# Performance work log

Hardware: AMD Instinct MI355X
Metric: run time of the kernel (lower is better)

## Reference

```python
import jax, jax.numpy as jnp
import numpy as np

POOL_SIZE = 7  # matches init kwarg pool_size


def setup_inputs() -> dict:
    key = jax.random.key(0)
    k1, k2 = jax.random.split(key, 2)
    H, W, C, N = 50, 64, 1024, 1000
    stride = 16
    shared_layers = jax.random.normal(k1, (1, H, W, C), dtype=jnp.float32)
    # ROIs in image coordinates (y1, x1, y2, x2), image ~ (H*stride, W*stride)
    img_h, img_w = float(H * stride), float(W * stride)
    u = jax.random.uniform(k2, (N, 4), dtype=jnp.float32)
    y1 = u[:, 0] * (img_h * 0.6)
    x1 = u[:, 1] * (img_w * 0.6)
    y2 = y1 + 32.0 + u[:, 2] * (img_h * 0.4 - 32.0)
    x2 = x1 + 32.0 + u[:, 3] * (img_w * 0.4 - 32.0)
    rois = jnp.stack([y1, x1, y2, x2], axis=1)
    return {"shared_layers": shared_layers, "rois": rois, "extractor_stride": stride}


def _crop_and_resize(img, boxes, cs):
    """TF tf.image.crop_and_resize (bilinear, extrapolation_value=0) for a single image.
    img: [H, W, C]; boxes: [N, 4] normalized (y1, x1, y2, x2); cs: crop size (>1).
    Returns [N, cs, cs, C]."""
    H, W, C = img.shape
    y1, x1, y2, x2 = boxes[:, 0], boxes[:, 1], boxes[:, 2], boxes[:, 3]
    i = jnp.arange(cs, dtype=boxes.dtype)
    # sample coordinates in source pixel space: [N, cs]
    ys = y1[:, None] * (H - 1) + i[None, :] * ((y2 - y1) * (H - 1) / (cs - 1))[:, None]
    xs = x1[:, None] * (W - 1) + i[None, :] * ((x2 - x1) * (W - 1) / (cs - 1))[:, None]
    valid_y = (ys >= 0) & (ys <= H - 1)
    valid_x = (xs >= 0) & (xs <= W - 1)
    y0f = jnp.floor(ys)
    x0f = jnp.floor(xs)
    wy = (ys - y0f)[:, :, None, None]   # [N, cs, 1, 1]
    wx = (xs - x0f)[:, None, :, None]   # [N, 1, cs, 1]
    y0 = jnp.clip(y0f.astype(jnp.int32), 0, H - 1)
    y1i = jnp.clip(y0 + 1, 0, H - 1)
    x0 = jnp.clip(x0f.astype(jnp.int32), 0, W - 1)
    x1i = jnp.clip(x0 + 1, 0, W - 1)

    def gather(yi, xi):  # -> [N, cs, cs, C]
        return img[yi[:, :, None], xi[:, None, :]]

    top = gather(y0, x0) * (1.0 - wx) + gather(y0, x1i) * wx
    bot = gather(y1i, x0) * (1.0 - wx) + gather(y1i, x1i) * wx
    out = top * (1.0 - wy) + bot * wy
    mask = (valid_y[:, :, None] & valid_x[:, None, :])[..., None]
    return jnp.where(mask, out, jnp.zeros((), dtype=img.dtype))


def reference(shared_layers, rois, extractor_stride):
    rois = rois / jnp.asarray(extractor_stride, dtype=rois.dtype)
    H, W = shared_layers.shape[1], shared_layers.shape[2]
    # normalize (y1/h, x1/w, y2/h, x2/w)
    boxes = rois / jnp.array([H, W, H, W], dtype=rois.dtype)
    cs = POOL_SIZE * 2  # pre_pool_size
    crops = _crop_and_resize(shared_layers[0], boxes, cs)  # [N, 14, 14, C]
    N, C = crops.shape[0], crops.shape[-1]
    # MaxPooling2D pool 2x2 stride 2 (14 even -> padding irrelevant)
    pooled = crops.reshape(N, POOL_SIZE, 2, POOL_SIZE, 2, C).max(axis=(2, 4))
    return jax.lax.stop_gradient(pooled.reshape(N, -1))
```

## Files before the change

### kernel.cpp

```cpp
#include <hip/hip_runtime.h>
#include <math.h>

namespace {

typedef float vf4 __attribute__((ext_vector_type(4)));

constexpr int kRowBytes = 64 * 1024 * 4;
constexpr int kColBytes = 1024 * 4;

__device__ __forceinline__ int rfl(int x) { return __builtin_amdgcn_readfirstlane(x); }

__device__ __forceinline__ vf4 splat4(float x) {
  vf4 v = {x, x, x, x};
  return v;
}

__global__ void roi_setup_kernel(const float* __restrict__ rois,
                                 const int* __restrict__ stride_p,
                                 int4* __restrict__ tab, int N) {
  const int t = blockIdx.x * 64 + threadIdx.x;
  if (t >= N * 7) return;
  const int n = t / 7;
  const int k = t - n * 7;

  const float s = (float)(*stride_p);
  const float by1 = rois[n * 4 + 0] / s / 50.0f;
  const float bx1 = rois[n * 4 + 1] / s / 64.0f;
  const float by2 = rois[n * 4 + 2] / s / 50.0f;
  const float bx2 = rois[n * 4 + 3] / s / 64.0f;
  const float stepy = (by2 - by1) * 49.0f / 13.0f;
  const float stepx = (bx2 - bx1) * 63.0f / 13.0f;

  const float ys0 = by1 * 49.0f + (float)(2 * k + 0) * stepy;
  const float ys1 = by1 * 49.0f + (float)(2 * k + 1) * stepy;
  const float vy0 = (ys0 >= 0.0f && ys0 <= 49.0f) ? 1.0f : 0.0f;
  const float vy1 = (ys1 >= 0.0f && ys1 <= 49.0f) ? 1.0f : 0.0f;
  const float yf0 = floorf(ys0), yf1 = floorf(ys1);
  const float wy0 = ys0 - yf0, wy1 = ys1 - yf1;
  const int r0 = min(max((int)yf0, 0), 49);
  const int r1 = min(r0 + 1, 49);
  const int r2 = min(max((int)yf1, 0), 49);
  const int r3 = min(r2 + 1, 49);
  tab[2 * t] = make_int4(r0 * kRowBytes, r1 * kRowBytes,
                         r2 * kRowBytes, r3 * kRowBytes);
  ((float4*)tab)[2 * t + 1] =
      make_float4((1.0f - wy0) * vy0, wy0 * vy0, (1.0f - wy1) * vy1, wy1 * vy1);

  const float xs0 = bx1 * 63.0f + (float)(2 * k + 0) * stepx;
  const float xs1 = bx1 * 63.0f + (float)(2 * k + 1) * stepx;
  const float vx0 = (xs0 >= 0.0f && xs0 <= 63.0f) ? 1.0f : 0.0f;
  const float vx1 = (xs1 >= 0.0f && xs1 <= 63.0f) ? 1.0f : 0.0f;
  const float xf0 = floorf(xs0), xf1 = floorf(xs1);
  const float wx0 = xs0 - xf0, wx1 = xs1 - xf1;
  const int c0 = min(max((int)xf0, 0), 63);
  const int c1 = min(c0 + 1, 63);
  const int c2 = min(max((int)xf1, 0), 63);
  const int c3 = min(c2 + 1, 63);
  const int xoff = N * 14;
  tab[xoff + 2 * t] = make_int4(c0 * kColBytes, c1 * kColBytes,
                                c2 * kColBytes, c3 * kColBytes);
  ((float4*)tab)[xoff + 2 * t + 1] =
      make_float4((1.0f - wx0) * vx0, wx0 * vx0, (1.0f - wx1) * vx1, wx1 * vx1);
}

__global__ __launch_bounds__(256) void roi_pool_tab(
    const float* __restrict__ img,
    const int4* __restrict__ tab, int N,
    float* __restrict__ out) {
  const int bid = blockIdx.x;
  const int chunk = gridDim.x >> 3;
  const int pos = ((gridDim.x & 7) == 0) ? ((bid & 7) * chunk + (bid >> 3)) : bid;
  const int n  = pos / 49;
  const int rr = pos - n * 49;
  const int py = rr / 7;
  const int px = rr - py * 7;
  const int c4 = threadIdx.x;

  const int yt = 2 * (n * 7 + py);
  const int xt = N * 14 + 2 * (n * 7 + px);
  const int4   yi = tab[yt];
  const float4 yw = ((const float4*)tab)[yt + 1];
  const int4   xi = tab[xt];
  const float4 xw = ((const float4*)tab)[xt + 1];

  const int r0 = rfl(yi.x), r1 = rfl(yi.y), r2 = rfl(yi.z), r3 = rfl(yi.w);
  const int c0 = rfl(xi.x), c1 = rfl(xi.y), c2 = rfl(xi.z), c3 = rfl(xi.w);

  const vf4 gy0 = splat4(yw.x), fy0 = splat4(yw.y);
  const vf4 gy1 = splat4(yw.z), fy1 = splat4(yw.w);
  const vf4 gx0 = splat4(xw.x), fx0 = splat4(xw.y);
  const vf4 gx1 = splat4(xw.z), fx1 = splat4(xw.w);

  const char* __restrict__ imgb = (const char*)img;
  const int coff = c4 * 16;

  const bool c2e0 = (c2 == c0), c2e1 = (c2 == c1);
  const bool c3e1 = (c3 == c1), c3e2 = (c3 == c2);

  auto rowblend = [&](int rB, vf4& b0, vf4& b1) {
    const vf4 q0 = *(const vf4*)(imgb + (rB + c0) + coff);
    const vf4 q1 = *(const vf4*)(imgb + (rB + c1) + coff);
    vf4 q2, q3;
    if (c2e0)      q2 = q0;
    else if (c2e1) q2 = q1;
    else           q2 = *(const vf4*)(imgb + (rB + c2) + coff);
    if (c3e1)      q3 = q1;
    else if (c3e2) q3 = q2;
    else           q3 = *(const vf4*)(imgb + (rB + c3) + coff);
    b0 = q0 * gx0 + q1 * fx0;
    b1 = q2 * gx1 + q3 * fx1;
  };

  vf4 b00, b01, b10, b11, b20, b21, b30, b31;
  rowblend(r0, b00, b01);
  if (r1 == r0) { b10 = b00; b11 = b01; }
  else rowblend(r1, b10, b11);
  if (r2 == r0)      { b20 = b00; b21 = b01; }
  else if (r2 == r1) { b20 = b10; b21 = b11; }
  else rowblend(r2, b20, b21);
  if (r3 == r1)      { b30 = b10; b31 = b11; }
  else if (r3 == r2) { b30 = b20; b31 = b21; }
  else rowblend(r3, b30, b31);

  vf4 m = b00 * gy0 + b10 * fy0;
  vf4 v = b01 * gy0 + b11 * fy0;
  m = __builtin_elementwise_max(m, v);
  v = b20 * gy1 + b30 * fy1;
  m = __builtin_elementwise_max(m, v);
  v = b21 * gy1 + b31 * fy1;
  m = __builtin_elementwise_max(m, v);

  __builtin_nontemporal_store(m, (vf4*)out + (size_t)pos * 256 + c4);
}

__device__ __forceinline__ float rflf(float x) {
  union { float f; int i; } u;
  u.f = x;
  u.i = __builtin_amdgcn_readfirstlane(u.i);
  return u.f;
}

__global__ __launch_bounds__(256) void roi_pool_kernel(
    const float* __restrict__ img, const float* __restrict__ rois,
    const int* __restrict__ stride_p, float* __restrict__ out) {
  const int bid = blockIdx.x;
  const int chunk = gridDim.x >> 3;
  const int pos = ((gridDim.x & 7) == 0) ? ((bid & 7) * chunk + (bid >> 3)) : bid;
  const int n  = pos / 49;
  const int rr = pos - n * 49;
  const int py = rr / 7;
  const int px = rr - py * 7;
  const int c4 = threadIdx.x;

  const float s = (float)(*stride_p);
  const float by1 = rois[n * 4 + 0] / s / 50.0f;
  const float bx1 = rois[n * 4 + 1] / s / 64.0f;
  const float by2 = rois[n * 4 + 2] / s / 50.0f;
  const float bx2 = rois[n * 4 + 3] / s / 64.0f;
  const float stepy = (by2 - by1) * 49.0f / 13.0f;
  const float stepx = (bx2 - bx1) * 63.0f / 13.0f;

  const float ys0 = by1 * 49.0f + (float)(2 * py + 0) * stepy;
  const float ys1 = by1 * 49.0f + (float)(2 * py + 1) * stepy;
  const float xs0 = bx1 * 63.0f + (float)(2 * px + 0) * stepx;
  const float xs1 = bx1 * 63.0f + (float)(2 * px + 1) * stepx;
  const float vy0 = (ys0 >= 0.0f && ys0 <= 49.0f) ? 1.0f : 0.0f;
  const float vy1 = (ys1 >= 0.0f && ys1 <= 49.0f) ? 1.0f : 0.0f;
  const float vx0 = (xs0 >= 0.0f && xs0 <= 63.0f) ? 1.0f : 0.0f;
  const float vx1 = (xs1 >= 0.0f && xs1 <= 63.0f) ? 1.0f : 0.0f;
  const float yf0 = floorf(ys0), yf1 = floorf(ys1);
  const float xf0 = floorf(xs0), xf1 = floorf(xs1);
  const float wy0 = ys0 - yf0, wy1 = ys1 - yf1;
  const float wx0 = xs0 - xf0, wx1 = xs1 - xf1;
  const int r0i = min(max((int)yf0, 0), 49);
  const int r2i = min(max((int)yf1, 0), 49);
  const int c0i = min(max((int)xf0, 0), 63);
  const int c2i = min(max((int)xf1, 0), 63);
  const int r0 = rfl(r0i), r1 = rfl(min(r0i + 1, 49));
  const int r2 = rfl(r2i), r3 = rfl(min(r2i + 1, 49));
  const int c0 = rfl(c0i), c1 = rfl(min(c0i + 1, 63));
  const int c2 = rfl(c2i), c3 = rfl(min(c2i + 1, 63));
  const vf4 gy0 = splat4(rflf((1.0f - wy0) * vy0));
  const vf4 fy0 = splat4(rflf(wy0 * vy0));
  const vf4 gy1 = splat4(rflf((1.0f - wy1) * vy1));
  const vf4 fy1 = splat4(rflf(wy1 * vy1));
  const vf4 gx0 = splat4(rflf((1.0f - wx0) * vx0));
  const vf4 fx0 = splat4(rflf(wx0 * vx0));
  const vf4 gx1 = splat4(rflf((1.0f - wx1) * vx1));
  const vf4 fx1 = splat4(rflf(wx1 * vx1));

  const vf4* __restrict__ img4 = (const vf4*)img;
  const bool c2e0 = (c2 == c0), c2e1 = (c2 == c1);
  const bool c3e1 = (c3 == c1), c3e2 = (c3 == c2);
  const int co0 = c0 * 256, co1 = c1 * 256, co2 = c2 * 256, co3 = c3 * 256;

  auto rowblend = [&](int r, vf4& b0, vf4& b1) {
    const vf4* rp = img4 + r * (64 * 256);
    const vf4 q0 = rp[co0 + c4];
    const vf4 q1 = rp[co1 + c4];
    vf4 q2, q3;
    if (c2e0)      q2 = q0;
    else if (c2e1) q2 = q1;
    else           q2 = rp[co2 + c4];
    if (c3e1)      q3 = q1;
    else if (c3e2) q3 = q2;
    else           q3 = rp[co3 + c4];
    b0 = q0 * gx0 + q1 * fx0;
    b1 = q2 * gx1 + q3 * fx1;
  };

  vf4 b00, b01, b10, b11, b20, b21, b30, b31;
  rowblend(r0, b00, b01);
  if (r1 == r0) { b10 = b00; b11 = b01; }
  else rowblend(r1, b10, b11);
  if (r2 == r0)      { b20 = b00; b21 = b01; }
  else if (r2 == r1) { b20 = b10; b21 = b11; }
  else rowblend(r2, b20, b21);
  if (r3 == r1)      { b30 = b10; b31 = b11; }
  else if (r3 == r2) { b30 = b20; b31 = b21; }
  else rowblend(r3, b30, b31);

  vf4 m = b00 * gy0 + b10 * fy0;
  vf4 v = b01 * gy0 + b11 * fy0;
  m = __builtin_elementwise_max(m, v);
  v = b20 * gy1 + b30 * fy1;
  m = __builtin_elementwise_max(m, v);
  v = b21 * gy1 + b31 * fy1;
  m = __builtin_elementwise_max(m, v);

  __builtin_nontemporal_store(m, (vf4*)out + (size_t)pos * 256 + c4);
}

}

extern "C" void kernel_launch(void* const* d_in, const int* in_sizes, int n_in,
                              void* d_out, int out_size, void* d_ws, size_t ws_size,
                              hipStream_t stream) {
  const float* img      = (const float*)d_in[0];
  const float* rois     = (const float*)d_in[1];
  const int*   stride_p = (const int*)d_in[2];
  float*       out      = (float*)d_out;

  const int N = in_sizes[1] / 4;
  const size_t tab_bytes = (size_t)N * 28 * 16;

  if (ws_size >= tab_bytes) {
    int4* tab = (int4*)d_ws;
    const int nt = N * 7;
    roi_setup_kernel<<<(nt + 63) / 64, 64, 0, stream>>>(rois, stride_p, tab, N);
    roi_pool_tab<<<N * 49, 256, 0, stream>>>(img, tab, N, out);
  } else {
    roi_pool_kernel<<<N * 49, 256, 0, stream>>>(img, rois, stride_p, out);
  }
}
```

Measured before the change: 98.80 us.

## Sort ROIs by vertical center to improve cache locality of feature-map gathers

Adds a single-block bitonic sort kernel that orders ROIs by quantized y-center and writes a permutation. The setup and pooling kernels process ROIs in sorted order, so concurrently running blocks read nearby feature-map rows, while outputs are still written to each ROI's original slot. This aims to improve L2/MALL hit rates on the 13 MB image. The cost is an extra serial single-block launch, an indirection load per block, and scattered output writes.

```diff
diff --git a/kernel.cpp b/kernel.cpp
--- a/kernel.cpp
+++ b/kernel.cpp
@@ -15,13 +15,49 @@
   return v;
 }
 
+__global__ __launch_bounds__(512) void roi_sort_kernel(
+    const float* __restrict__ rois, const int* __restrict__ stride_p,
+    int* __restrict__ perm, int N) {
+  __shared__ unsigned sk[1024];
+  const int tid = threadIdx.x;
+  const float s = (float)(*stride_p);
+
+  for (int i = tid; i < 1024; i += 512) {
+    unsigned key = 0xFFFFFFFFu;
+    if (i < N) {
+      const float yc = (rois[i * 4 + 0] + rois[i * 4 + 2]) * 0.5f / s;
+      int q = (int)(yc * (1024.0f / 50.0f));
+      q = min(max(q, 0), 1023);
+      key = ((unsigned)q << 10) | (unsigned)i;
+    }
+    sk[i] = key;
+  }
+  __syncthreads();
+
+  for (unsigned k = 2; k <= 1024; k <<= 1) {
+    for (unsigned j = k >> 1; j > 0; j >>= 1) {
+      const unsigned t = tid;
+      const unsigned i1 = ((t & ~(j - 1)) << 1) | (t & (j - 1));
+      const unsigned i2 = i1 | j;
+      const unsigned a = sk[i1], b = sk[i2];
+      const bool up = ((i1 & k) == 0);
+      if ((a > b) == up) { sk[i1] = b; sk[i2] = a; }
+      __syncthreads();
+    }
+  }
+
+  for (int i = tid; i < N; i += 512) perm[i] = (int)(sk[i] & 1023u);
+}
+
 __global__ void roi_setup_kernel(const float* __restrict__ rois,
                                  const int* __restrict__ stride_p,
+                                 const int* __restrict__ perm,
                                  int4* __restrict__ tab, int N) {
   const int t = blockIdx.x * 64 + threadIdx.x;
   if (t >= N * 7) return;
-  const int n = t / 7;
-  const int k = t - n * 7;
+  const int sn = t / 7;
+  const int k = t - sn * 7;
+  const int n = perm[sn];
 
   const float s = (float)(*stride_p);
   const float by1 = rois[n * 4 + 0] / s / 50.0f;
@@ -65,19 +101,21 @@
 
 __global__ __launch_bounds__(256) void roi_pool_tab(
     const float* __restrict__ img,
-    const int4* __restrict__ tab, int N,
+    const int4* __restrict__ tab,
+    const int* __restrict__ perm, int N,
     float* __restrict__ out) {
   const int bid = blockIdx.x;
   const int chunk = gridDim.x >> 3;
   const int pos = ((gridDim.x & 7) == 0) ? ((bid & 7) * chunk + (bid >> 3)) : bid;
-  const int n  = pos / 49;
-  const int rr = pos - n * 49;
+  const int sn = pos / 49;
+  const int rr = pos - sn * 49;
   const int py = rr / 7;
   const int px = rr - py * 7;
   const int c4 = threadIdx.x;
 
-  const int yt = 2 * (n * 7 + py);
-  const int xt = N * 14 + 2 * (n * 7 + px);
+  const int yt = 2 * (sn * 7 + py);
+  const int xt = N * 14 + 2 * (sn * 7 + px);
+  const int    n  = perm[sn];
   const int4   yi = tab[yt];
   const float4 yw = ((const float4*)tab)[yt + 1];
   const int4   xi = tab[xt];
@@ -130,7 +168,7 @@
   v = b21 * gy1 + b31 * fy1;
   m = __builtin_elementwise_max(m, v);
 
-  __builtin_nontemporal_store(m, (vf4*)out + (size_t)pos * 256 + c4);
+  __builtin_nontemporal_store(m, (vf4*)out + ((size_t)n * 49 + rr) * 256 + c4);
 }
 
 __device__ __forceinline__ float rflf(float x) {
@@ -242,13 +280,16 @@
   float*       out      = (float*)d_out;
 
   const int N = in_sizes[1] / 4;
-  const size_t tab_bytes = (size_t)N * 28 * 16;
-
-  if (ws_size >= tab_bytes) {
-    int4* tab = (int4*)d_ws;
-    const int nt = N * 7;
-    roi_setup_kernel<<<(nt + 63) / 64, 64, 0, stream>>>(rois, stride_p, tab, N);
-    roi_pool_tab<<<N * 49, 256, 0, stream>>>(img, tab, N, out);
+  const size_t tab_bytes  = (size_t)N * 28 * 16;
+  const size_t perm_bytes = (size_t)((N + 63) & ~63) * sizeof(int);
+
+  if (ws_size >= tab_bytes + perm_bytes && N <= 1024) {
+    int4* tab  = (int4*)d_ws;
+    int*  perm = (int*)((char*)d_ws + tab_bytes);
+    roi_sort_kernel<<<1, 512, 0, stream>>>(rois, stride_p, perm, N);
+    roi_setup_kernel<<<(N * 7 + 63) / 64, 64, 0, stream>>>(rois, stride_p, perm,
+                                                           tab, N);
+    roi_pool_tab<<<N * 49, 256, 0, stream>>>(img, tab, perm, N, out);
   } else {
     roi_pool_kernel<<<N * 49, 256, 0, stream>>>(img, rois, stride_p, out);
   }
```

Measured after the change: 86.30 us (median of 2 runs). 12.7% less time.
